# Kernel tuning notes

Hardware: AMD Instinct MI355X
Metric: run time of the kernel (lower is better)

The kernel has to match this reference:

```python
import jax, jax.numpy as jnp
import numpy as np

# Circuit dimensions: B batch, N sum nodes (rows), C child nodes (cols), NSE stored edges.
B, N, C, NSE = 256, 8192, 32768, 524288


def setup_inputs() -> dict:
    key = jax.random.key(0)
    k1, k2, k3, k4 = jax.random.split(key, 4)
    # child log-likelihoods (output of child_layer.log_likelihood_of_nodes), [B, C]
    child_ll = jax.random.normal(k1, (B, C), dtype=jnp.float32) - 2.0
    # BCOO .data of the (unnormalized) log weights, [NSE]
    log_w_data = jax.random.normal(k2, (NSE,), dtype=jnp.float32)
    # BCOO indices[:, 0]: parent sum-node row of each edge. Guarantee every row
    # appears at least once so no node is empty (log(0) avoided), then sort
    # (matching .sort_indices() row-major ordering).
    rows = jnp.sort(jnp.concatenate([
        jnp.arange(N, dtype=jnp.int32),
        jax.random.randint(k3, (NSE - N,), 0, N, dtype=jnp.int32),
    ]))
    # BCOO indices[:, 1]: child node column of each edge
    cols = jax.random.randint(k4, (NSE,), 0, C, dtype=jnp.int32)
    return {"child_ll": child_ll, "log_w_data": log_w_data,
            "rows": rows, "cols": cols, "n_nodes": N}


def reference(child_ll, log_w_data, rows, cols, n_nodes):
    # log normalization constants per node (max-stabilized, as in
    # SparseSumLayer.log_normalization_constants)
    m = log_w_data.max()
    z = m + jnp.log(jax.ops.segment_sum(jnp.exp(log_w_data - m), rows,
                                        num_segments=n_nodes))  # [N]
    # per-edge: exp(log_w + child_ll[col])  (as in log_likelihood_of_nodes_single)
    vals = jnp.exp(log_w_data[None, :] + child_ll[:, cols])        # [B, NSE]
    # row-wise sparse sum (BCOO .sum(1).todense())
    summed = jax.ops.segment_sum(vals.T, rows, num_segments=n_nodes).T  # [B, N]
    # normalized log-likelihood of each sum node
    return jnp.log(summed) - z[None, :]
```

## Files before the change

kernel.cpp:

```cpp
#include <hip/hip_runtime.h>
#include <hip/hip_bf16.h>

#define BB   256
#define NN   8192
#define CC   32768
#define NSE_ 524288
#define GB   32
#define PREP_BLOCKS ((NSE_ + 64 + 255) / 256)
#define TP_TILE 128
#define TP_BLOCKS ((CC / TP_TILE) * 8)

typedef float v2f __attribute__((ext_vector_type(2)));

__device__ __forceinline__ unsigned int f2bf_rne(float f) {
    unsigned int u = __float_as_uint(f);
    return (u + 0x7fffu + ((u >> 16) & 1u)) >> 16;
}

__global__ __launch_bounds__(256) void prep_transpose_kernel(
    const float* __restrict__ lw, const int* __restrict__ rows,
    const int* __restrict__ cols, const float* __restrict__ ll,
    uint2* __restrict__ cw, int* __restrict__ rs,
    unsigned int* __restrict__ cet32) {
    int bid = blockIdx.x;
    int t = threadIdx.x;
    if (bid < PREP_BLOCKS) {
        int e = bid * 256 + t;
        if (e < NSE_) {
            cw[e] = make_uint2((unsigned)cols[e],
                               __float_as_uint(__expf(lw[e])));
            if (e == 0) { rs[0] = 0; rs[NN] = NSE_; }
            else if (rows[e] != rows[e - 1]) rs[rows[e]] = e;
        } else if (e < NSE_ + 64) {
            cw[e] = make_uint2(0u, 0u);
        }
        return;
    }
    bid -= PREP_BLOCKS;
    int g = bid & 7;
    int ct = bid >> 3;
    int c0 = ct * TP_TILE, b0 = g * GB;
    __shared__ float tile[TP_TILE][GB + 1];
    #pragma unroll
    for (int k = 0; k < 4; ++k) {
        int idx = t + 256 * k;
        int bl = idx >> 5;
        int c4 = idx & 31;
        const float4 v = *reinterpret_cast<const float4*>(
            ll + (size_t)(b0 + bl) * CC + c0 + c4 * 4);
        tile[c4 * 4 + 0][bl] = v.x;
        tile[c4 * 4 + 1][bl] = v.y;
        tile[c4 * 4 + 2][bl] = v.z;
        tile[c4 * 4 + 3][bl] = v.w;
    }
    __syncthreads();
    size_t baseu = ((size_t)g * CC + c0) * 16;
    #pragma unroll
    for (int k = 0; k < 8; ++k) {
        int u = t + 256 * k;
        int c = u >> 4, b2 = (u & 15) * 2;
        unsigned int lo = f2bf_rne(__expf(tile[c][b2]));
        unsigned int hi = f2bf_rne(__expf(tile[c][b2 + 1]));
        cet32[baseu + u] = lo | (hi << 16);
    }
}

__global__ __launch_bounds__(256) void sum_rows_kernel(
    const uint2* __restrict__ cw, const int* __restrict__ rs,
    const uint4* __restrict__ cet, float* __restrict__ out) {
    __shared__ float lds_out[32][17];
    int g = blockIdx.x & 7;
    int ntile = blockIdx.x >> 3;
    int n0 = ntile * 16;
    int wv = threadIdx.x >> 6;
    int lane = threadIdx.x & 63;
    int grp = lane >> 2;
    int bq = lane & 3;
    const uint4* slice = cet + (size_t)g * CC * 4;

    for (int r = 0; r < 4; ++r) {
        int n = n0 + wv * 4 + r;
        int s = __builtin_amdgcn_readfirstlane(rs[n]);
        int t = __builtin_amdgcn_readfirstlane(rs[n + 1]);
        v2f acc[4];
        acc[0] = 0.f; acc[1] = 0.f; acc[2] = 0.f; acc[3] = 0.f;
        float zs = 0.f;
        int eb = s;
        for (; eb + 64 <= t; eb += 64) {
            #pragma unroll
            for (int j = 0; j < 4; ++j) {
                uint2 p = cw[eb + j * 16 + grp];
                float w = __uint_as_float(p.y);
                uint4 u = slice[(p.x << 2) | bq];
                v2f w2; w2.x = w; w2.y = w;
                v2f g0, g1, g2, g3;
                g0.x = __uint_as_float(u.x << 16);
                g0.y = __uint_as_float(u.x & 0xffff0000u);
                g1.x = __uint_as_float(u.y << 16);
                g1.y = __uint_as_float(u.y & 0xffff0000u);
                g2.x = __uint_as_float(u.z << 16);
                g2.y = __uint_as_float(u.z & 0xffff0000u);
                g3.x = __uint_as_float(u.w << 16);
                g3.y = __uint_as_float(u.w & 0xffff0000u);
                acc[0] += w2 * g0;
                acc[1] += w2 * g1;
                acc[2] += w2 * g2;
                acc[3] += w2 * g3;
                zs += w;
            }
        }
        if (eb < t) {
            #pragma unroll
            for (int j = 0; j < 4; ++j) {
                int e = eb + j * 16 + grp;
                uint2 p = cw[e];
                float w = (e < t) ? __uint_as_float(p.y) : 0.f;
                uint4 u = slice[(p.x << 2) | bq];
                v2f w2; w2.x = w; w2.y = w;
                v2f g0, g1, g2, g3;
                g0.x = __uint_as_float(u.x << 16);
                g0.y = __uint_as_float(u.x & 0xffff0000u);
                g1.x = __uint_as_float(u.y << 16);
                g1.y = __uint_as_float(u.y & 0xffff0000u);
                g2.x = __uint_as_float(u.z << 16);
                g2.y = __uint_as_float(u.z & 0xffff0000u);
                g3.x = __uint_as_float(u.w << 16);
                g3.y = __uint_as_float(u.w & 0xffff0000u);
                acc[0] += w2 * g0;
                acc[1] += w2 * g1;
                acc[2] += w2 * g2;
                acc[3] += w2 * g3;
                zs += w;
            }
        }
        #pragma unroll
        for (int off = 4; off <= 32; off <<= 1) {
            #pragma unroll
            for (int k = 0; k < 4; ++k) {
                acc[k].x += __shfl_xor(acc[k].x, off);
                acc[k].y += __shfl_xor(acc[k].y, off);
            }
            zs += __shfl_xor(zs, off);
        }
        if (grp == 0) {
            float lz = __logf(zs);
            #pragma unroll
            for (int k = 0; k < 4; ++k) {
                lds_out[bq * 8 + k * 2 + 0][wv * 4 + r] = __logf(acc[k].x) - lz;
                lds_out[bq * 8 + k * 2 + 1][wv * 4 + r] = __logf(acc[k].y) - lz;
            }
        }
    }
    __syncthreads();
    if (threadIdx.x < 128) {
        int bl = threadIdx.x >> 2, ch = threadIdx.x & 3;
        float4 v = make_float4(lds_out[bl][ch * 4 + 0], lds_out[bl][ch * 4 + 1],
                               lds_out[bl][ch * 4 + 2], lds_out[bl][ch * 4 + 3]);
        *reinterpret_cast<float4*>(
            out + (size_t)(g * GB + bl) * NN + n0 + ch * 4) = v;
    }
}

extern "C" void kernel_launch(void* const* d_in, const int* in_sizes, int n_in,
                              void* d_out, int out_size, void* d_ws, size_t ws_size,
                              hipStream_t stream) {
    const float* child_ll = (const float*)d_in[0];
    const float* log_w    = (const float*)d_in[1];
    const int*   rows     = (const int*)  d_in[2];
    const int*   cols     = (const int*)  d_in[3];
    float* out = (float*)d_out;

    char* ws = (char*)d_ws;
    uint2*        cwp = (uint2*)ws;
    int*          rs  = (int*)(ws + (size_t)6 * 1024 * 1024);
    unsigned int* cet = (unsigned int*)(ws + (size_t)8 * 1024 * 1024);

    prep_transpose_kernel<<<PREP_BLOCKS + TP_BLOCKS, 256, 0, stream>>>(
        log_w, rows, cols, child_ll, cwp, rs, cet);
    sum_rows_kernel<<<(NN / 16) * 8, 256, 0, stream>>>(
        cwp, rs, (const uint4*)cet, out);
}
```

Baseline: 131.9 us.

## Stage edge list through LDS with prefetch; convert to bf16 before transpose

In the main kernel, each wave now loads 64 (col, weight) pairs with one coalesced load into an LDS staging buffer and prefetches the next chunk while working on the current one. This replaces the redundant per-group global loads and merges the full-chunk and tail paths into one loop. The transpose stage now exps and packs to bf16 before writing to shared memory, using 64-column tiles and vector uint4 stores. It removes duplicate global traffic and latency at the cost of extra LDS round-trips per chunk.

```diff
diff --git a/kernel.cpp b/kernel.cpp
--- a/kernel.cpp
+++ b/kernel.cpp
@@ -7,14 +7,16 @@
 #define NSE_ 524288
 #define GB   32
 #define PREP_BLOCKS ((NSE_ + 64 + 255) / 256)
-#define TP_TILE 128
-#define TP_BLOCKS ((CC / TP_TILE) * 8)
+#define TP_BLOCKS   ((CC / 64) * 8)
 
 typedef float v2f __attribute__((ext_vector_type(2)));
 
 __device__ __forceinline__ unsigned int f2bf_rne(float f) {
     unsigned int u = __float_as_uint(f);
     return (u + 0x7fffu + ((u >> 16) & 1u)) >> 16;
+}
+__device__ __forceinline__ unsigned int pack2bf(float lo, float hi) {
+    return f2bf_rne(lo) | (f2bf_rne(hi) << 16);
 }
 
 __global__ __launch_bounds__(256) void prep_transpose_kernel(
@@ -39,35 +41,38 @@
     bid -= PREP_BLOCKS;
     int g = bid & 7;
     int ct = bid >> 3;
-    int c0 = ct * TP_TILE, b0 = g * GB;
-    __shared__ float tile[TP_TILE][GB + 1];
-    #pragma unroll
-    for (int k = 0; k < 4; ++k) {
-        int idx = t + 256 * k;
-        int bl = idx >> 5;
-        int c4 = idx & 31;
-        const float4 v = *reinterpret_cast<const float4*>(
-            ll + (size_t)(b0 + bl) * CC + c0 + c4 * 4);
-        tile[c4 * 4 + 0][bl] = v.x;
-        tile[c4 * 4 + 1][bl] = v.y;
-        tile[c4 * 4 + 2][bl] = v.z;
-        tile[c4 * 4 + 3][bl] = v.w;
+    int c0 = ct * 64, b0 = g * GB;
+    __shared__ unsigned int tile_u[16][68];
+    {
+        int c4 = t & 15, bp = t >> 4;
+        const float4 fa = *reinterpret_cast<const float4*>(
+            ll + (size_t)(b0 + 2 * bp + 0) * CC + c0 + 4 * c4);
+        const float4 fb = *reinterpret_cast<const float4*>(
+            ll + (size_t)(b0 + 2 * bp + 1) * CC + c0 + 4 * c4);
+        uint4 u;
+        u.x = pack2bf(__expf(fa.x), __expf(fb.x));
+        u.y = pack2bf(__expf(fa.y), __expf(fb.y));
+        u.z = pack2bf(__expf(fa.z), __expf(fb.z));
+        u.w = pack2bf(__expf(fa.w), __expf(fb.w));
+        *reinterpret_cast<uint4*>(&tile_u[bp][4 * c4]) = u;
     }
     __syncthreads();
-    size_t baseu = ((size_t)g * CC + c0) * 16;
-    #pragma unroll
-    for (int k = 0; k < 8; ++k) {
-        int u = t + 256 * k;
-        int c = u >> 4, b2 = (u & 15) * 2;
-        unsigned int lo = f2bf_rne(__expf(tile[c][b2]));
-        unsigned int hi = f2bf_rne(__expf(tile[c][b2 + 1]));
-        cet32[baseu + u] = lo | (hi << 16);
+    {
+        int c = t >> 2, q = t & 3;
+        uint4 o;
+        o.x = tile_u[4 * q + 0][c];
+        o.y = tile_u[4 * q + 1][c];
+        o.z = tile_u[4 * q + 2][c];
+        o.w = tile_u[4 * q + 3][c];
+        size_t base_u = ((size_t)g * CC + c0) * 16;
+        *reinterpret_cast<uint4*>(cet32 + base_u + c * 16 + 4 * q) = o;
     }
 }
 
 __global__ __launch_bounds__(256) void sum_rows_kernel(
     const uint2* __restrict__ cw, const int* __restrict__ rs,
     const uint4* __restrict__ cet, float* __restrict__ out) {
+    __shared__ uint2 stage[4][64];
     __shared__ float lds_out[32][17];
     int g = blockIdx.x & 7;
     int ntile = blockIdx.x >> 3;
@@ -77,6 +82,7 @@
     int grp = lane >> 2;
     int bq = lane & 3;
     const uint4* slice = cet + (size_t)g * CC * 4;
+    uint2* st = stage[wv];
 
     for (int r = 0; r < 4; ++r) {
         int n = n0 + wv * 4 + r;
@@ -85,36 +91,15 @@
         v2f acc[4];
         acc[0] = 0.f; acc[1] = 0.f; acc[2] = 0.f; acc[3] = 0.f;
         float zs = 0.f;
-        int eb = s;
-        for (; eb + 64 <= t; eb += 64) {
+        uint2 v = cw[s + lane];
+        for (int eb = s; eb < t; eb += 64) {
+            if (eb + lane >= t) v.y = 0u;
+            st[lane] = v;
+            if (eb + 64 < t) v = cw[eb + 64 + lane];
             #pragma unroll
             for (int j = 0; j < 4; ++j) {
-                uint2 p = cw[eb + j * 16 + grp];
+                uint2 p = st[j * 16 + grp];
                 float w = __uint_as_float(p.y);
-                uint4 u = slice[(p.x << 2) | bq];
-                v2f w2; w2.x = w; w2.y = w;
-                v2f g0, g1, g2, g3;
-                g0.x = __uint_as_float(u.x << 16);
-                g0.y = __uint_as_float(u.x & 0xffff0000u);
-                g1.x = __uint_as_float(u.y << 16);
-                g1.y = __uint_as_float(u.y & 0xffff0000u);
-                g2.x = __uint_as_float(u.z << 16);
-                g2.y = __uint_as_float(u.z & 0xffff0000u);
-                g3.x = __uint_as_float(u.w << 16);
-                g3.y = __uint_as_float(u.w & 0xffff0000u);
-                acc[0] += w2 * g0;
-                acc[1] += w2 * g1;
-                acc[2] += w2 * g2;
-                acc[3] += w2 * g3;
-                zs += w;
-            }
-        }
-        if (eb < t) {
-            #pragma unroll
-            for (int j = 0; j < 4; ++j) {
-                int e = eb + j * 16 + grp;
-                uint2 p = cw[e];
-                float w = (e < t) ? __uint_as_float(p.y) : 0.f;
                 uint4 u = slice[(p.x << 2) | bq];
                 v2f w2; w2.x = w; w2.y = w;
                 v2f g0, g1, g2, g3;
```

Measured after the change: 128.1 us. -2.9%, faster.
